# Kernel optimization log

Hardware: AMD Instinct MI355X
Metric: run time of the kernel (lower is better)

Reference implementation:

```python
import jax, jax.numpy as jnp
import numpy as np

K, N, GROUP = 4096, 12288, 64
M = 4096  # tokens (batch*seq)


def setup_inputs() -> dict:
    key = jax.random.key(0)
    k1, k2, k3, k4, k5 = jax.random.split(key, 5)
    input = jax.random.normal(k1, (M, K), dtype=jnp.float32)
    qweight = jax.random.randint(k2, (K, N), 0, 4, dtype=jnp.int32)  # int2 codes in [0,4)
    scale = jax.random.uniform(k3, (K // GROUP, N), dtype=jnp.float32)
    zp = jax.random.normal(k4, (K // GROUP, N), dtype=jnp.float32)
    bias = jax.random.normal(k5, (N,), dtype=jnp.float32)
    return {"input": input, "qweight": qweight, "scale": scale, "zp": zp, "bias": bias}


def reference(input, qweight, scale, zp, bias):
    # Group-wise asymmetric dequant: W[k,n] = q[k,n]*scale[k//g,n] + zp[k//g,n]
    G = K // GROUP
    q = qweight.astype(input.dtype).reshape(G, GROUP, N)
    w = q * scale[:, None, :] + zp[:, None, :]          # [G, g, N]
    w = w.reshape(K, N)
    out = input @ w + bias[None, :]                      # [M, N]
    return out
```

## Files before the change

kernel.cpp:

```cpp
#include <hip/hip_runtime.h>
#include <hip/hip_bf16.h>

#define Mdim 4096
#define Kdim 4096
#define Ndim 12288

typedef __attribute__((ext_vector_type(8))) short short8;
typedef __attribute__((ext_vector_type(4))) float floatx4;
typedef __attribute__((ext_vector_type(4))) unsigned short ushortx4;
typedef __attribute__((ext_vector_type(8))) unsigned short ushortx8;

static __device__ __forceinline__ unsigned short f2bf(float x) {
    __hip_bfloat16 h = __float2bfloat16(x);
    return __builtin_bit_cast(unsigned short, h);
}

static __device__ __forceinline__ void gload_lds16(const unsigned short* g, unsigned short* l) {
    __builtin_amdgcn_global_load_lds(
        (const __attribute__((address_space(1))) unsigned int*)g,
        (__attribute__((address_space(3))) unsigned int*)l,
        16, 0, 0);
}

__global__ void __launch_bounds__(256)
dequant_transpose(const int* __restrict__ Q, const float* __restrict__ S,
                  const float* __restrict__ Z, unsigned short* __restrict__ Wt)
{
    __shared__ unsigned short Ls[64][72];
    const int t  = threadIdx.x;
    const int k0 = blockIdx.x * 64;
    const int n0 = blockIdx.y * 64;
    const int g  = k0 >> 6;

    const int nc  = (t & 15) * 4;
    const int kr0 = t >> 4;
    const floatx4 s4 = *reinterpret_cast<const floatx4*>(&S[(size_t)g * Ndim + n0 + nc]);
    const floatx4 z4 = *reinterpret_cast<const floatx4*>(&Z[(size_t)g * Ndim + n0 + nc]);

    #pragma unroll
    for (int i = 0; i < 4; ++i) {
        const int kr = kr0 + i * 16;
        const int4 q = *reinterpret_cast<const int4*>(&Q[(size_t)(k0 + kr) * Ndim + n0 + nc]);
        Ls[nc + 0][kr] = f2bf(fmaf((float)q.x, s4.x, z4.x));
        Ls[nc + 1][kr] = f2bf(fmaf((float)q.y, s4.y, z4.y));
        Ls[nc + 2][kr] = f2bf(fmaf((float)q.z, s4.z, z4.z));
        Ls[nc + 3][kr] = f2bf(fmaf((float)q.w, s4.w, z4.w));
    }
    __syncthreads();

    const int n  = t >> 2;
    const int kc = (t & 3) * 16;
    const ushortx8 a = *reinterpret_cast<const ushortx8*>(&Ls[n][kc]);
    const ushortx8 b = *reinterpret_cast<const ushortx8*>(&Ls[n][kc + 8]);
    unsigned short* dst = &Wt[(size_t)(n0 + n) * Kdim + k0 + kc];
    *reinterpret_cast<ushortx8*>(dst)     = a;
    *reinterpret_cast<ushortx8*>(dst + 8) = b;
}

__global__ void __launch_bounds__(256)
xconv(const float* __restrict__ X, unsigned short* __restrict__ Xw)
{
    const size_t i = ((size_t)blockIdx.x * 256 + threadIdx.x) * 8;
    const floatx4 a = *reinterpret_cast<const floatx4*>(&X[i]);
    const floatx4 b = *reinterpret_cast<const floatx4*>(&X[i + 4]);
    ushortx8 w;
    w[0] = f2bf(a.x); w[1] = f2bf(a.y); w[2] = f2bf(a.z); w[3] = f2bf(a.w);
    w[4] = f2bf(b.x); w[5] = f2bf(b.y); w[6] = f2bf(b.z); w[7] = f2bf(b.w);
    *reinterpret_cast<ushortx8*>(&Xw[i]) = w;
}

__global__ void __launch_bounds__(256)
gemm_bf16(const unsigned short* __restrict__ A, const unsigned short* __restrict__ B,
          const float* __restrict__ bias, float* __restrict__ O)
{
    __shared__ unsigned short As[128 * 64];
    __shared__ unsigned short Bs[128 * 64];

    const int nblk = Ndim / 128;
    const int gsz  = 8 * nblk;
    const int grp  = blockIdx.x / gsz;
    const int r    = blockIdx.x % gsz;
    const int m0   = (grp * 8 + (r & 7)) * 128;
    const int n0   = (r >> 3) * 128;

    const int t    = threadIdx.x;
    const int wave = t >> 6;
    const int lane = t & 63;
    const int wm   = (wave & 1) * 64;
    const int wn   = (wave >> 1) * 64;
    const int lrow = lane & 15;
    const int quad = lane >> 4;

    const int srow = lane >> 3;
    const int scol = (lane & 7) * 8;
    const unsigned short* Ag = &A[(size_t)(m0 + wave * 32 + srow) * Kdim + scol];
    const unsigned short* Bg = &B[(size_t)(n0 + wave * 32 + srow) * Kdim + scol];
    unsigned short* AsB = &As[(wave * 32) * 64];
    unsigned short* BsB = &Bs[(wave * 32) * 64];

    floatx4 acc[4][4];
    #pragma unroll
    for (int i = 0; i < 4; ++i)
        #pragma unroll
        for (int j = 0; j < 4; ++j)
            acc[i][j] = floatx4{0.f, 0.f, 0.f, 0.f};

    for (int k0 = 0; k0 < Kdim; k0 += 64) {
        #pragma unroll
        for (int it = 0; it < 4; ++it) {
            gload_lds16(Ag + (size_t)(it * 8) * Kdim + k0, AsB + it * 8 * 64);
            gload_lds16(Bg + (size_t)(it * 8) * Kdim + k0, BsB + it * 8 * 64);
        }
        __syncthreads();

        #pragma unroll
        for (int kk = 0; kk < 64; kk += 32) {
            short8 af[4], bfr[4];
            #pragma unroll
            for (int i = 0; i < 4; ++i)
                af[i] = *reinterpret_cast<const short8*>(
                    &As[(wm + i * 16 + lrow) * 64 + kk + quad * 8]);
            #pragma unroll
            for (int j = 0; j < 4; ++j)
                bfr[j] = *reinterpret_cast<const short8*>(
                    &Bs[(wn + j * 16 + lrow) * 64 + kk + quad * 8]);
            #pragma unroll
            for (int i = 0; i < 4; ++i)
                #pragma unroll
                for (int j = 0; j < 4; ++j)
                    acc[i][j] = __builtin_amdgcn_mfma_f32_16x16x32_bf16(
                        af[i], bfr[j], acc[i][j], 0, 0, 0);
        }
        __syncthreads();
    }

    #pragma unroll
    for (int j = 0; j < 4; ++j) {
        const int col = n0 + wn + j * 16 + lrow;
        const float bv = bias[col];
        #pragma unroll
        for (int i = 0; i < 4; ++i) {
            const int rbase = m0 + wm + i * 16 + quad * 4;
            #pragma unroll
            for (int rr = 0; rr < 4; ++rr)
                O[(size_t)(rbase + rr) * Ndim + col] = acc[i][j][rr] + bv;
        }
    }
}

__global__ void __launch_bounds__(256)
w2a16_gemm_fb(const float* __restrict__ X, const int* __restrict__ Q,
              const float* __restrict__ S, const float* __restrict__ Z,
              const float* __restrict__ bias, float* __restrict__ O)
{
    __shared__ unsigned short As[128][72];
    __shared__ unsigned short Bs[128][72];
    const int t  = threadIdx.x;
    const int n0 = blockIdx.x * 128;
    const int m0 = blockIdx.y * 128;
    const int wave = t >> 6, lane = t & 63;
    const int wm = (wave & 1) * 64, wn = (wave >> 1) * 64;
    const int lrow = lane & 15, quad = lane >> 4;
    floatx4 acc[4][4];
    #pragma unroll
    for (int i = 0; i < 4; ++i)
        #pragma unroll
        for (int j = 0; j < 4; ++j) acc[i][j] = floatx4{0.f, 0.f, 0.f, 0.f};
    const int a_row0 = t >> 4, a_c = (t & 15) * 4;
    const int b_n = t & 127, b_k0 = (t >> 7) * 32;
    for (int k0 = 0; k0 < Kdim; k0 += 64) {
        #pragma unroll
        for (int i = 0; i < 8; ++i) {
            const int row = a_row0 + i * 16;
            const floatx4 v = *reinterpret_cast<const floatx4*>(
                &X[(size_t)(m0 + row) * Kdim + k0 + a_c]);
            ushortx4 w;
            w.x = f2bf(v.x); w.y = f2bf(v.y); w.z = f2bf(v.z); w.w = f2bf(v.w);
            *reinterpret_cast<ushortx4*>(&As[row][a_c]) = w;
        }
        const int g = k0 >> 6;
        const float s = S[(size_t)g * Ndim + n0 + b_n];
        const float z = Z[(size_t)g * Ndim + n0 + b_n];
        #pragma unroll
        for (int i = 0; i < 8; ++i) {
            const int kk = b_k0 + i * 4;
            const int* qp = &Q[(size_t)(k0 + kk) * Ndim + n0 + b_n];
            ushortx4 w;
            w.x = f2bf(fmaf((float)qp[0],                s, z));
            w.y = f2bf(fmaf((float)qp[(size_t)Ndim],     s, z));
            w.z = f2bf(fmaf((float)qp[(size_t)2 * Ndim], s, z));
            w.w = f2bf(fmaf((float)qp[(size_t)3 * Ndim], s, z));
            *reinterpret_cast<ushortx4*>(&Bs[b_n][kk]) = w;
        }
        __syncthreads();
        #pragma unroll
        for (int kk = 0; kk < 64; kk += 32) {
            short8 af[4], bfr[4];
            #pragma unroll
            for (int i = 0; i < 4; ++i)
                af[i] = *reinterpret_cast<const short8*>(&As[wm + i * 16 + lrow][kk + quad * 8]);
            #pragma unroll
            for (int j = 0; j < 4; ++j)
                bfr[j] = *reinterpret_cast<const short8*>(&Bs[wn + j * 16 + lrow][kk + quad * 8]);
            #pragma unroll
            for (int i = 0; i < 4; ++i)
                #pragma unroll
                for (int j = 0; j < 4; ++j)
                    acc[i][j] = __builtin_amdgcn_mfma_f32_16x16x32_bf16(af[i], bfr[j], acc[i][j], 0, 0, 0);
        }
        __syncthreads();
    }
    #pragma unroll
    for (int j = 0; j < 4; ++j) {
        const int col = n0 + wn + j * 16 + lrow;
        const float bv = bias[col];
        #pragma unroll
        for (int i = 0; i < 4; ++i) {
            const int rbase = m0 + wm + i * 16 + quad * 4;
            #pragma unroll
            for (int rr = 0; rr < 4; ++rr)
                O[(size_t)(rbase + rr) * Ndim + col] = acc[i][j][rr] + bv;
        }
    }
}

extern "C" void kernel_launch(void* const* d_in, const int* in_sizes, int n_in,
                              void* d_out, int out_size, void* d_ws, size_t ws_size,
                              hipStream_t stream) {
    const float* X  = (const float*)d_in[0];
    const int*   Q  = (const int*)d_in[1];
    const float* S  = (const float*)d_in[2];
    const float* Z  = (const float*)d_in[3];
    const float* Bi = (const float*)d_in[4];
    float* O = (float*)d_out;

    const size_t wt_bytes = (size_t)Kdim * Ndim * 2;
    const size_t xw_bytes = (size_t)Mdim * Kdim * 2;

    if (ws_size >= wt_bytes + xw_bytes) {
        unsigned short* Wt = (unsigned short*)d_ws;
        unsigned short* Xw = (unsigned short*)((char*)d_ws + wt_bytes);

        dim3 g1(Kdim / 64, Ndim / 64);
        hipLaunchKernelGGL(dequant_transpose, g1, dim3(256), 0, stream, Q, S, Z, Wt);

        const int xblocks = (Mdim * Kdim) / (256 * 8);
        hipLaunchKernelGGL(xconv, dim3(xblocks), dim3(256), 0, stream, X, Xw);

        const int nblocks = (Mdim / 128) * (Ndim / 128);
        hipLaunchKernelGGL(gemm_bf16, dim3(nblocks), dim3(256), 0, stream, Xw, Wt, Bi, O);
    } else {
        dim3 grid(Ndim / 128, Mdim / 128);
        hipLaunchKernelGGL(w2a16_gemm_fb, grid, dim3(256), 0, stream, X, Q, S, Z, Bi, O);
    }
}
```

Measured before the change: 945.7 us.

## Swizzle GEMM LDS tiles and batch dequant-transpose over four K-groups per block

The GEMM kernel now applies an XOR swizzle to the 16-byte column chunks of the A and B LDS tiles, both when the global-to-LDS loads write them and when the MFMA fragments read them back. This targets LDS bank conflicts on the fragment reads. The dequant-transpose kernel now has each block process four consecutive 64-row K groups. Each thread writes four packed bf16 values per LDS store instead of scattered single shorts, and the grid shrinks by a factor of four, trading lower launch and scatter overhead for fewer blocks and extra barriers.

```diff
diff --git a/kernel.cpp b/kernel.cpp
--- a/kernel.cpp
+++ b/kernel.cpp
@@ -7,6 +7,7 @@
 
 typedef __attribute__((ext_vector_type(8))) short short8;
 typedef __attribute__((ext_vector_type(4))) float floatx4;
+typedef __attribute__((ext_vector_type(4))) int intx4;
 typedef __attribute__((ext_vector_type(4))) unsigned short ushortx4;
 typedef __attribute__((ext_vector_type(8))) unsigned short ushortx8;
 
@@ -27,34 +28,42 @@
                   const float* __restrict__ Z, unsigned short* __restrict__ Wt)
 {
     __shared__ unsigned short Ls[64][72];
-    const int t  = threadIdx.x;
-    const int k0 = blockIdx.x * 64;
-    const int n0 = blockIdx.y * 64;
-    const int g  = k0 >> 6;
-
-    const int nc  = (t & 15) * 4;
-    const int kr0 = t >> 4;
-    const floatx4 s4 = *reinterpret_cast<const floatx4*>(&S[(size_t)g * Ndim + n0 + nc]);
-    const floatx4 z4 = *reinterpret_cast<const floatx4*>(&Z[(size_t)g * Ndim + n0 + nc]);
-
-    #pragma unroll
-    for (int i = 0; i < 4; ++i) {
-        const int kr = kr0 + i * 16;
-        const int4 q = *reinterpret_cast<const int4*>(&Q[(size_t)(k0 + kr) * Ndim + n0 + nc]);
-        Ls[nc + 0][kr] = f2bf(fmaf((float)q.x, s4.x, z4.x));
-        Ls[nc + 1][kr] = f2bf(fmaf((float)q.y, s4.y, z4.y));
-        Ls[nc + 2][kr] = f2bf(fmaf((float)q.z, s4.z, z4.z));
-        Ls[nc + 3][kr] = f2bf(fmaf((float)q.w, s4.w, z4.w));
-    }
-    __syncthreads();
-
-    const int n  = t >> 2;
-    const int kc = (t & 3) * 16;
-    const ushortx8 a = *reinterpret_cast<const ushortx8*>(&Ls[n][kc]);
-    const ushortx8 b = *reinterpret_cast<const ushortx8*>(&Ls[n][kc + 8]);
-    unsigned short* dst = &Wt[(size_t)(n0 + n) * Kdim + k0 + kc];
-    *reinterpret_cast<ushortx8*>(dst)     = a;
-    *reinterpret_cast<ushortx8*>(dst + 8) = b;
+    const int t     = threadIdx.x;
+    const int kbase = blockIdx.x * 256;
+    const int n0    = blockIdx.y * 64;
+    const int tn = t & 15, tk = t >> 4;
+    const int nc = tn * 4;
+    const int n_out  = t >> 2;
+    const int kc_out = (t & 3) * 16;
+
+    #pragma unroll
+    for (int s = 0; s < 4; ++s) {
+        const int k0 = kbase + s * 64;
+        const int g  = k0 >> 6;
+        const floatx4 s4 = *reinterpret_cast<const floatx4*>(&S[(size_t)g * Ndim + n0 + nc]);
+        const floatx4 z4 = *reinterpret_cast<const floatx4*>(&Z[(size_t)g * Ndim + n0 + nc]);
+        intx4 q[4];
+        #pragma unroll
+        for (int r = 0; r < 4; ++r)
+            q[r] = *reinterpret_cast<const intx4*>(&Q[(size_t)(k0 + tk * 4 + r) * Ndim + n0 + nc]);
+        if (s) __syncthreads();
+        #pragma unroll
+        for (int j = 0; j < 4; ++j) {
+            const float sv = s4[j], zv = z4[j];
+            ushortx4 w;
+            w.x = f2bf(fmaf((float)q[0][j], sv, zv));
+            w.y = f2bf(fmaf((float)q[1][j], sv, zv));
+            w.z = f2bf(fmaf((float)q[2][j], sv, zv));
+            w.w = f2bf(fmaf((float)q[3][j], sv, zv));
+            *reinterpret_cast<ushortx4*>(&Ls[nc + j][tk * 4]) = w;
+        }
+        __syncthreads();
+        const ushortx8 a = *reinterpret_cast<const ushortx8*>(&Ls[n_out][kc_out]);
+        const ushortx8 b = *reinterpret_cast<const ushortx8*>(&Ls[n_out][kc_out + 8]);
+        unsigned short* dst = &Wt[(size_t)(n0 + n_out) * Kdim + k0 + kc_out];
+        *reinterpret_cast<ushortx8*>(dst)     = a;
+        *reinterpret_cast<ushortx8*>(dst + 8) = b;
+    }
 }
 
 __global__ void __launch_bounds__(256)
@@ -90,9 +99,10 @@
     const int wn   = (wave >> 1) * 64;
     const int lrow = lane & 15;
     const int quad = lane >> 4;
+    const int lsw  = lrow & 7;
 
     const int srow = lane >> 3;
-    const int scol = (lane & 7) * 8;
+    const int scol = ((lane & 7) ^ srow) * 8;
     const unsigned short* Ag = &A[(size_t)(m0 + wave * 32 + srow) * Kdim + scol];
     const unsigned short* Bg = &B[(size_t)(n0 + wave * 32 + srow) * Kdim + scol];
     unsigned short* AsB = &As[(wave * 32) * 64];
@@ -115,15 +125,16 @@
 
         #pragma unroll
         for (int kk = 0; kk < 64; kk += 32) {
+            const int cphys = (((kk >> 3) + quad) ^ lsw) * 8;
             short8 af[4], bfr[4];
             #pragma unroll
             for (int i = 0; i < 4; ++i)
                 af[i] = *reinterpret_cast<const short8*>(
-                    &As[(wm + i * 16 + lrow) * 64 + kk + quad * 8]);
+                    &As[(wm + i * 16 + lrow) * 64 + cphys]);
             #pragma unroll
             for (int j = 0; j < 4; ++j)
                 bfr[j] = *reinterpret_cast<const short8*>(
-                    &Bs[(wn + j * 16 + lrow) * 64 + kk + quad * 8]);
+                    &Bs[(wn + j * 16 + lrow) * 64 + cphys]);
             #pragma unroll
             for (int i = 0; i < 4; ++i)
                 #pragma unroll
@@ -241,7 +252,7 @@
         unsigned short* Wt = (unsigned short*)d_ws;
         unsigned short* Xw = (unsigned short*)((char*)d_ws + wt_bytes);
 
-        dim3 g1(Kdim / 64, Ndim / 64);
+        dim3 g1(Kdim / 256, Ndim / 64);
         hipLaunchKernelGGL(dequant_transpose, g1, dim3(256), 0, stream, Q, S, Z, Wt);
 
         const int xblocks = (Mdim * Kdim) / (256 * 8);
```

Result: faster. 853.8 us (-9.7%).
